# Optimization experiments

Hardware: AMD Instinct MI355X
Metric: run time of the kernel (lower is better)

The kernel has to match this reference:

```python
import jax, jax.numpy as jnp
import numpy as np
from jax import lax

RADIUS = 0.15
K = 32          # num_neighbors
S = 1024        # num_centers
GROUPS = 8      # GroupNorm groups
EPS = 1e-5


def furthest_point_sample(xyz, n_samples):
    # xyz: [B, N, 3] -> indices [B, n_samples] (sequential FPS, start at index 0)
    B, N, _ = xyz.shape
    def step(carry, _):
        min_d, far = carry                      # [B,N], [B]
        sel = jnp.take_along_axis(xyz, far[:, None, None], axis=1)  # [B,1,3]
        d = jnp.sum((xyz - sel) ** 2, axis=-1)  # [B,N]
        min_d = jnp.minimum(min_d, d)
        nxt = jnp.argmax(min_d, axis=-1).astype(jnp.int32)
        return (min_d, nxt), far
    init = (jnp.full((B, N), jnp.inf, dtype=xyz.dtype), jnp.zeros((B,), jnp.int32))
    _, idxs = lax.scan(step, init, None, length=n_samples)  # [n_samples, B]
    return idxs.T  # [B, n_samples]


def ball_query(centers, points, radius, k):
    # centers: [B,3,S], points: [B,3,N] -> neighbor indices [B,S,k]
    B = points.shape[0]
    N = points.shape[-1]
    d2 = jnp.sum((centers[:, :, :, None] - points[:, :, None, :]) ** 2, axis=1)  # [B,S,N]
    valid = d2 < radius * radius
    order = jnp.where(valid, jnp.arange(N, dtype=jnp.int32), jnp.int32(N))
    topk = jnp.sort(order, axis=-1)[..., :k]            # first-k in-ball indices (CUDA ball_query order)
    first = topk[..., :1]
    idx = jnp.where(topk < N, topk, first)              # pad shortfall with first in-ball point
    idx = jnp.where(idx == N, 0, idx)                   # empty ball -> index 0
    return idx


def grouping(x, idx):
    # x: [B,C,N], idx: [B,S,k] -> [B,C,S,k]
    B, C, N = x.shape
    _, s, k = idx.shape
    flat = idx.reshape(B, 1, s * k)
    g = jnp.take_along_axis(x, jnp.broadcast_to(flat, (B, C, s * k)), axis=2)
    return g.reshape(B, C, s, k)


def group_norm(x, gamma, beta):
    # x: [B,C,S,K], GroupNorm(GROUPS)
    B, C, s, k = x.shape
    xg = x.reshape(B, GROUPS, C // GROUPS, s, k)
    mu = jnp.mean(xg, axis=(2, 3, 4), keepdims=True)
    var = jnp.var(xg, axis=(2, 3, 4), keepdims=True)
    xn = ((xg - mu) * lax.rsqrt(var + EPS)).reshape(B, C, s, k)
    return xn * gamma[None, :, None, None] + beta[None, :, None, None]


def mlp_layer(x, w, b, gamma, beta):
    # 1x1 Conv2d + GroupNorm + swish; x: [B,C,S,K], w: [O,C]
    y = jnp.einsum('bcsk,oc->bosk', x, w) + b[None, :, None, None]
    y = group_norm(y, gamma, beta)
    return y * jax.nn.sigmoid(y)


def setup_inputs() -> dict:
    key = jax.random.key(0)
    ks = jax.random.split(key, 20)
    B, C_IN, N = 8, 128, 4096
    features = jax.random.normal(ks[0], (B, C_IN, N), jnp.float32)
    coords = jax.random.uniform(ks[1], (B, 3, N), jnp.float32)
    time_emb = jax.random.normal(ks[2], (B, 64, N), jnp.float32)
    style = jax.random.normal(ks[3], (B, 64), jnp.float32)
    chans = [C_IN + 3, 128, 128, 256]
    inp = dict(features=features, coords=coords, time_emb=time_emb, style=style)
    for i in range(3):
        ci, co = chans[i], chans[i + 1]
        inp[f'w{i+1}'] = jax.random.normal(ks[4 + 4 * i], (co, ci), jnp.float32) / np.sqrt(ci)
        inp[f'b{i+1}'] = jnp.zeros((co,), jnp.float32)
        inp[f'g{i+1}'] = jnp.ones((co,), jnp.float32)
        inp[f'be{i+1}'] = jnp.zeros((co,), jnp.float32)
    return inp


def reference(features, coords, time_emb, style,
              w1, b1, g1, be1, w2, b2, g2, be2, w3, b3, g3, be3):
    # FPS -> center coords
    fps_idx = furthest_point_sample(coords.transpose(0, 2, 1), S)       # [B,S]
    B = coords.shape[0]
    centers = jnp.take_along_axis(coords, jnp.broadcast_to(fps_idx[:, None, :], (B, 3, S)), axis=2)  # [B,3,S]
    # Ball query + grouping (include_coordinates=True)
    nidx = ball_query(centers, coords, RADIUS, K)                       # [B,S,K]
    ncoords = grouping(coords, nidx) - centers[:, :, :, None]           # [B,3,S,K]
    nfeat = jnp.concatenate([ncoords, grouping(features, nidx)], axis=1)  # [B,3+C,S,K]
    # SharedMLP (1x1 conv + GN(8) + swish) x3, then max over neighbors
    x = mlp_layer(nfeat, w1, b1, g1, be1)
    x = mlp_layer(x, w2, b2, g2, be2)
    x = mlp_layer(x, w3, b3, g3, be3)
    out = jnp.max(x, axis=-1)                                           # [B,256,S]
    return out, centers, time_emb[:, :, :S], style
```

## Files before the change

### kernel.cpp

```cpp
#include <hip/hip_runtime.h>
#include <hip/hip_bf16.h>

#define BATCH 8
#define NPTS 4096
#define NS   1024
#define NK   32
#define CIN  128
#define C1PAD 160
#define O1   128
#define O3   256
#define MTOT 32768
#define GN_EPS 1e-5f
#define SREP 64

typedef float f32x4 __attribute__((ext_vector_type(4)));
typedef float f32x2 __attribute__((ext_vector_type(2)));
typedef short s16x8 __attribute__((ext_vector_type(8)));
typedef short s16x4 __attribute__((ext_vector_type(4)));
typedef unsigned long long u64;
typedef u64 u64x2 __attribute__((ext_vector_type(2)));

static __device__ __forceinline__ unsigned short f2bf(float f){
  unsigned u = __float_as_uint(f);
  u += 0x7fffu + ((u >> 16) & 1u);
  return (unsigned short)(u >> 16);
}
static __device__ __forceinline__ float bf2f(unsigned short h){
  return __uint_as_float(((unsigned)h) << 16);
}
static __device__ __forceinline__ float exact_d2(float ax,float ay,float az,float bx,float by,float bz){
  float dx=__fadd_rn(ax,-bx), dy=__fadd_rn(ay,-by), dz=__fadd_rn(az,-bz);
  return __fadd_rn(__fadd_rn(__fmul_rn(dx,dx),__fmul_rn(dy,dy)),__fmul_rn(dz,dz));
}
static __device__ __forceinline__ unsigned wave_umax_dpp(unsigned v){
  unsigned o;
  o = (unsigned)__builtin_amdgcn_update_dpp(0, (int)v, 0x111, 0xf, 0xf, true); v = (o>v)?o:v;
  o = (unsigned)__builtin_amdgcn_update_dpp(0, (int)v, 0x112, 0xf, 0xf, true); v = (o>v)?o:v;
  o = (unsigned)__builtin_amdgcn_update_dpp(0, (int)v, 0x114, 0xf, 0xf, true); v = (o>v)?o:v;
  o = (unsigned)__builtin_amdgcn_update_dpp(0, (int)v, 0x118, 0xf, 0xf, true); v = (o>v)?o:v;
  o = (unsigned)__builtin_amdgcn_update_dpp(0, (int)v, 0x142, 0xf, 0xf, true); v = (o>v)?o:v;
  o = (unsigned)__builtin_amdgcn_update_dpp(0, (int)v, 0x143, 0xf, 0xf, true); v = (o>v)?o:v;
  return v;
}
static __device__ __forceinline__ float wave_fsum_dpp(float v){
  int o;
  o=__builtin_amdgcn_update_dpp(0,__float_as_int(v),0x111,0xf,0xf,true); v+=__int_as_float(o);
  o=__builtin_amdgcn_update_dpp(0,__float_as_int(v),0x112,0xf,0xf,true); v+=__int_as_float(o);
  o=__builtin_amdgcn_update_dpp(0,__float_as_int(v),0x114,0xf,0xf,true); v+=__int_as_float(o);
  o=__builtin_amdgcn_update_dpp(0,__float_as_int(v),0x118,0xf,0xf,true); v+=__int_as_float(o);
  o=__builtin_amdgcn_update_dpp(0,__float_as_int(v),0x142,0xf,0xf,true); v+=__int_as_float(o);
  o=__builtin_amdgcn_update_dpp(0,__float_as_int(v),0x143,0xf,0xf,true); v+=__int_as_float(o);
  return v;
}
static __device__ __forceinline__ float fast_sigmoid(float x){
  return __builtin_amdgcn_rcpf(1.0f + __expf(-x));
}
static __device__ __forceinline__ void stats_sum(const float* __restrict__ stats,
                                                 int layer,int b,int g,float& s1,float& s2){
  const float2* p = (const float2*)(stats + (size_t)(((layer*BATCH+b)*8+g)*SREP)*2);
  float a=0.f, q=0.f;
  #pragma unroll
  for(int r=0;r<SREP;++r){ float2 v=p[r]; a+=v.x; q+=v.y; }
  s1=a; s2=q;
}

#define FPS_BLOCKS 8
#define FT_BASE    8
#define FT_BLOCKS  128
#define ZP_BASE    136
#define ZP_BLOCKS  8
#define WP_BASE    144
#define WP_BLOCKS  130
#define MS_BASE    274
#define MS_BLOCKS  32
#define TOTAL_BLOCKS 306
#define WP_TASKS   (8704 + 3*BATCH*8*SREP*2)

__global__ __launch_bounds__(256) void k_fused(
    const float* __restrict__ coords, const float* __restrict__ features,
    const float* __restrict__ time_emb, const float* __restrict__ style,
    const float* __restrict__ w1, const float* __restrict__ w2, const float* __restrict__ w3,
    float* __restrict__ centers, float* __restrict__ out_time, float* __restrict__ out_style,
    unsigned short* __restrict__ featT, unsigned short* __restrict__ wfrag,
    float* __restrict__ stats){
  union U {
    struct { float4 lc[NPTS];
             unsigned long long red[2][4] __attribute__((aligned(16)));
             float cx_[NS]; float cy_[NS]; float cz_[NS]; } fps;
    float tile[64][65];
  };
  __shared__ U sm;
  const int blk = blockIdx.x;
  const int t = threadIdx.x;

  if(blk < FPS_BLOCKS){
    const int b = blk;
    const float* cb = coords + (size_t)b*3*NPTS;
    const int lane = t & 63, wid = t >> 6;
    f32x2 px2[8],py2[8],pz2[8],md2[8];
    #pragma unroll
    for(int i=0;i<8;++i){
      int p0 = t + (2*i)*256;
      px2[i]=(f32x2){cb[p0],cb[p0+256]};
      py2[i]=(f32x2){cb[NPTS+p0],cb[NPTS+p0+256]};
      pz2[i]=(f32x2){cb[2*NPTS+p0],cb[2*NPTS+p0+256]};
      md2[i]=(f32x2){3.4e38f,3.4e38f};
      sm.fps.lc[p0]     = make_float4(px2[i].x, py2[i].x, pz2[i].x, 0.f);
      sm.fps.lc[p0+256] = make_float4(px2[i].y, py2[i].y, pz2[i].y, 0.f);
    }
    float ax=cb[0], ay=cb[NPTS], az=cb[2*NPTS];
    if(t==0){ sm.fps.cx_[0]=ax; sm.fps.cy_[0]=ay; sm.fps.cz_[0]=az; }
    __syncthreads();
    for(int it=1; it<NS; ++it){
      {
        #pragma clang fp contract(off)
        f32x2 axv={ax,ax}, ayv={ay,ay}, azv={az,az};
        #pragma unroll
        for(int i=0;i<8;++i){
          f32x2 dx=px2[i]-axv, dy=py2[i]-ayv, dz=pz2[i]-azv;
          f32x2 d = dx*dx + dy*dy + dz*dz;
          md2[i]=__builtin_elementwise_min(md2[i],d);
        }
      }
      f32x2 t01=__builtin_elementwise_max(md2[0],md2[1]);
      f32x2 t23=__builtin_elementwise_max(md2[2],md2[3]);
      f32x2 t45=__builtin_elementwise_max(md2[4],md2[5]);
      f32x2 t67=__builtin_elementwise_max(md2[6],md2[7]);
      f32x2 ta=__builtin_elementwise_max(t01,t23);
      f32x2 tb=__builtin_elementwise_max(t45,t67);
      f32x2 tc=__builtin_elementwise_max(ta,tb);
      float bmax=fmaxf(tc.x,tc.y);
      unsigned bvb=(unsigned)__builtin_amdgcn_readlane((int)wave_umax_dpp(__float_as_uint(bmax)),63);
      unsigned cand=0u;
      #pragma unroll
      for(int s=15;s>=0;--s){
        float mv = (s&1)? md2[s>>1].y : md2[s>>1].x;
        cand = (__float_as_uint(mv)==bvb) ? ~(unsigned)(s*256+t) : cand;
      }
      unsigned mc = wave_umax_dpp(cand);
      const int buf=it&1;
      if(lane==63) sm.fps.red[buf][wid] = ((u64)bvb<<32) | mc;
      __syncthreads();
      u64x2 r0 = *(const u64x2*)&sm.fps.red[buf][0];
      u64x2 r1 = *(const u64x2*)&sm.fps.red[buf][2];
      u64 a0 = r0.x>r0.y?r0.x:r0.y;
      u64 a1 = r1.x>r1.y?r1.x:r1.y;
      u64 w  = a0>a1?a0:a1;
      unsigned idx = ~(unsigned)w;
      float4 c4 = sm.fps.lc[idx];
      ax=c4.x; ay=c4.y; az=c4.z;
      if(t==0){ sm.fps.cx_[it]=ax; sm.fps.cy_[it]=ay; sm.fps.cz_[it]=az; }
    }
    __syncthreads();
    for(int i=t;i<NS;i+=256){
      centers[(size_t)(b*3+0)*NS+i]=sm.fps.cx_[i];
      centers[(size_t)(b*3+1)*NS+i]=sm.fps.cy_[i];
      centers[(size_t)(b*3+2)*NS+i]=sm.fps.cz_[i];
    }
    return;
  }

  if(blk < ZP_BASE){
    const int pb = blk - FT_BASE;
    for(int j=0;j<8;++j){
      int tid = pb*8 + j;
      int bb = tid>>7, r = tid&127, ct = r>>6, pt = r&63;
      int c0 = ct*64, p0 = pt*64;
      #pragma unroll
      for(int i=0;i<16;++i){
        int c = (t>>6)*16 + i;
        sm.tile[c][t&63] = features[((size_t)bb*CIN + c0 + c)*NPTS + p0 + (t&63)];
      }
      __syncthreads();
      #pragma unroll
      for(int i=0;i<16;++i){
        int pl = (t>>6)*16 + i;
        featT[((size_t)bb*NPTS + p0 + pl)*C1PAD + c0 + (t&63)] = f2bf(sm.tile[t&63][pl]);
      }
      __syncthreads();
    }
    return;
  }

  if(blk < WP_BASE){
    const int zb = blk - ZP_BASE;
    s16x8 z = (s16x8){0,0,0,0,0,0,0,0};
    #pragma unroll 4
    for(int i=0;i<64;++i){
      int q = zb*16384 + i*256 + t;
      int bb = q>>14, rem = q&16383, r = rem>>2, c8 = (rem&3)*8;
      *(s16x8*)&featT[((size_t)bb*NPTS + r)*C1PAD + 128 + c8] = z;
    }
    return;
  }

  if(blk < MS_BASE){
    int task = (blk - WP_BASE)*256 + t;
    if(task >= WP_TASKS) return;
    if(task >= 8704){
      stats[task - 8704] = 0.f;
      return;
    }
    int layer, of, cs, ln, ncs; size_t base;
    if(task < 2560){ layer=0; ncs=5; base=0;     int r=task;      of=r/320; r%=320; cs=r>>6; ln=r&63; }
    else if(task < 4608){ layer=1; ncs=4; base=20480; int r=task-2560; of=r>>8; r&=255; cs=r>>6; ln=r&63; }
    else { layer=2; ncs=4; base=36864; int r=task-4608; of=r>>8; r&=255; cs=r>>6; ln=r&63; }
    int o = of*16 + (ln&15);
    s16x8 vals;
    #pragma unroll
    for(int i=0;i<8;++i){
      int c = cs*32 + (ln>>4)*8 + i;
      float v = 0.f;
      if(layer==0){
        if(c<128) v = w1[o*131 + c + 3];
        else if(c<131) v = w1[o*131 + (c-128)];
      } else if(layer==1){
        if(c<128) v = w2[o*128 + c];
      } else {
        if(c<128) v = w3[o*128 + c];
      }
      vals[i]=(short)f2bf(v);
    }
    *(s16x8*)&wfrag[base + ((size_t)(of*ncs + cs)*64 + ln)*8] = vals;
    return;
  }

  {
    const int mb = blk - MS_BASE;
    #pragma unroll 4
    for(int i=0;i<16;++i){
      int q = mb*4096 + i*256 + t;
      int f = q*4;
      int bb = f>>16, c = (f>>10)&63, s = f&1023;
      *(float4*)&out_time[f] = *(const float4*)&time_emb[((size_t)bb*64 + c)*NPTS + s];
    }
    if(mb==0){ out_style[t]=style[t]; out_style[256+t]=style[256+t]; }
  }
}

__global__ __launch_bounds__(256) void k_ballq(const float* __restrict__ coords,
                                               const float* __restrict__ centers,
                                               int* __restrict__ nidx){
  const int gw = (blockIdx.x*256 + threadIdx.x) >> 6;
  const int lane = threadIdx.x & 63;
  const int wl = (threadIdx.x >> 6);
  const int b = gw >> 10, s = gw & (NS-1);
  const float* cb = coords + (size_t)b*3*NPTS;
  const float cx = centers[(size_t)(b*3+0)*NS+s];
  const float cy = centers[(size_t)(b*3+1)*NS+s];
  const float cz = centers[(size_t)(b*3+2)*NS+s];
  __shared__ int slots[4][NK];
  int cnt = 0;
  for(int base=0; base<NPTS && cnt<NK; base+=64){
    int p = base + lane;
    float d2 = exact_d2(cb[p], cb[NPTS+p], cb[2*NPTS+p], cx,cy,cz);
    bool valid = d2 < 0.0225f;
    unsigned long long mask = __ballot(valid);
    int pos = cnt + (int)__popcll(mask & ((1ull<<lane)-1ull));
    if(valid && pos < NK) slots[wl][pos] = p;
    cnt += (int)__popcll(mask);
  }
  __syncthreads();
  int first = slots[wl][0];
  if(lane < NK){
    int v = (lane < cnt) ? slots[wl][lane] : first;
    nidx[((size_t)b*NS + s)*NK + lane] = v;
  }
}

__global__ __launch_bounds__(256) void k_gemm1(const unsigned short* __restrict__ featT,
    const int* __restrict__ nidx, const float* __restrict__ coords,
    const float* __restrict__ centers, const unsigned short* __restrict__ wfrag,
    const float* __restrict__ bias, unsigned short* __restrict__ yout,
    float* __restrict__ stats){
  const int b=blockIdx.y, mt=blockIdx.x;
  const int m0=mt*64;
  const int t=threadIdx.x, lane=t&63, wid=t>>6;
  __shared__ unsigned short xs[64][168];
  __shared__ unsigned short ys[64][136];
  __shared__ int pidx[64];
  __shared__ float cenS[2][3];
  __shared__ float wsum[2][8][4];
  if(t<64) pidx[t]=nidx[(size_t)b*MTOT + m0 + t];
  if(t>=64 && t<70){ int u=t-64; int j=u/3, c=u%3; cenS[j][c]=centers[((size_t)b*3+c)*NS + (m0>>5)+j]; }
  __syncthreads();
  for(int q=t;q<1280;q+=256){
    int r=q&63, ch=q>>6;
    *(s16x8*)&xs[r][ch*8] = *(const s16x8*)&featT[((size_t)b*NPTS + pidx[r])*C1PAD + ch*8];
  }
  __syncthreads();
  if(t<64){
    int p=pidx[t]; int sj=t>>5;
    float n0=__fadd_rn(coords[((size_t)b*3+0)*NPTS+p],-cenS[sj][0]);
    float n1=__fadd_rn(coords[((size_t)b*3+1)*NPTS+p],-cenS[sj][1]);
    float n2=__fadd_rn(coords[((size_t)b*3+2)*NPTS+p],-cenS[sj][2]);
    s16x4 nc={(short)f2bf(n0),(short)f2bf(n1),(short)f2bf(n2),0};
    *(s16x4*)&xs[t][128]=nc;
  }
  __syncthreads();
  f32x4 acc[8];
  #pragma unroll
  for(int i=0;i<8;++i) acc[i]=(f32x4){0.f,0.f,0.f,0.f};
  const unsigned short* xrow=&xs[wid*16+(lane&15)][0];
  #pragma unroll
  for(int cs=0;cs<5;++cs){
    s16x8 bfv=*(const s16x8*)&xrow[cs*32+(lane>>4)*8];
    #pragma unroll
    for(int of=0;of<8;++of){
      s16x8 afv=*(const s16x8*)&wfrag[((size_t)(of*5+cs)*64+lane)*8];
      acc[of]=__builtin_amdgcn_mfma_f32_16x16x32_bf16(afv,bfv,acc[of],0,0,0);
    }
  }
  #pragma unroll
  for(int of=0;of<8;++of){
    float ls=0.f,lq=0.f;
    int obase=of*16+((lane>>4)<<2);
    #pragma unroll
    for(int r=0;r<4;++r){
      float y=acc[of][r]+bias[obase+r];
      ys[wid*16+(lane&15)][obase+r]=f2bf(y);
      ls+=y; lq+=y*y;
    }
    ls=wave_fsum_dpp(ls); lq=wave_fsum_dpp(lq);
    if(lane==63){ wsum[0][of][wid]=ls; wsum[1][of][wid]=lq; }
  }
  __syncthreads();
  for(int q=t;q<1024;q+=256){
    int r=q&63, ch=q>>6;
    *(s16x8*)&yout[((size_t)b*MTOT+m0+r)*O1 + ch*8] = *(const s16x8*)&ys[r][ch*8];
  }
  if(t<8){
    float s1v=wsum[0][t][0]+wsum[0][t][1]+wsum[0][t][2]+wsum[0][t][3];
    float s2v=wsum[1][t][0]+wsum[1][t][1]+wsum[1][t][2]+wsum[1][t][3];
    int rep = mt & (SREP-1);
    atomicAdd(&stats[(((0*BATCH+b)*8+t)*SREP+rep)*2+0],s1v);
    atomicAdd(&stats[(((0*BATCH+b)*8+t)*SREP+rep)*2+1],s2v);
  }
}

template<int LAYER>
__global__ __launch_bounds__(256) void k_gemm23(const unsigned short* __restrict__ xin,
    const unsigned short* __restrict__ wfrag, const float* __restrict__ bias,
    const float* __restrict__ stats, const float* __restrict__ gprev,
    const float* __restrict__ beprev, unsigned short* __restrict__ yout,
    float* __restrict__ ymm, float* __restrict__ statsOut){
  const int b=blockIdx.y, mt=blockIdx.x;
  const int m0=mt*64;
  const int t=threadIdx.x, lane=t&63, wid=t>>6;
  __shared__ unsigned short xs[64][136];
  __shared__ unsigned short ys[64][136];
  __shared__ float lsc[CIN], lsh[CIN];
  __shared__ float wsum[2][8][4];
  if(t<CIN){
    int g = t>>4;
    const float cnt = 16.0f*NS*NK;
    float s1,s2; stats_sum(stats, LAYER-1, b, g, s1, s2);
    float mu=s1/cnt, var=s2/cnt-mu*mu;
    float sc=gprev[t]*rsqrtf(var+GN_EPS);
    lsc[t]=sc; lsh[t]=beprev[t]-mu*sc;
  }
  __syncthreads();
  for(int q=t;q<1024;q+=256){
    int r=q&63, ch=q>>6;
    s16x8 v = *(const s16x8*)&xin[((size_t)b*MTOT + m0 + r)*CIN + ch*8];
    s16x8 o;
    #pragma unroll
    for(int i=0;i<8;++i){
      int c=ch*8+i;
      float x = bf2f((unsigned short)v[i]);
      x = x*lsc[c] + lsh[c];
      o[i]=(short)f2bf(x*fast_sigmoid(x));
    }
    *(s16x8*)&xs[r][ch*8]=o;
  }
  __syncthreads();
  const unsigned short* xrow=&xs[wid*16+(lane&15)][0];
  s16x8 bfv[4];
  #pragma unroll
  for(int cs=0;cs<4;++cs) bfv[cs]=*(const s16x8*)&xrow[cs*32+(lane>>4)*8];
  const int NPH=(LAYER==2)?2:1;
  #pragma unroll
  for(int ph=0; ph<NPH; ++ph){
    f32x4 acc[8];
    #pragma unroll
    for(int i=0;i<8;++i) acc[i]=(f32x4){0.f,0.f,0.f,0.f};
    #pragma unroll
    for(int cs=0;cs<4;++cs){
      #pragma unroll
      for(int of=0;of<8;++of){
        int ofg=ph*8+of;
        s16x8 afv=*(const s16x8*)&wfrag[((size_t)(ofg*4+cs)*64+lane)*8];
        acc[of]=__builtin_amdgcn_mfma_f32_16x16x32_bf16(afv,bfv[cs],acc[of],0,0,0);
      }
    }
    #pragma unroll
    for(int of=0;of<8;++of){
      float ls=0.f,lq=0.f;
      int lobase=of*16+((lane>>4)<<2);
      #pragma unroll
      for(int r=0;r<4;++r){
        float y=acc[of][r]+bias[ph*128+lobase+r];
        ys[wid*16+(lane&15)][lobase+r]=f2bf(y);
        ls+=y; lq+=y*y;
      }
      ls=wave_fsum_dpp(ls); lq=wave_fsum_dpp(lq);
      if(lane==63){ wsum[0][of][wid]=ls; wsum[1][of][wid]=lq; }
    }
    __syncthreads();
    if constexpr(LAYER==1){
      for(int q=t;q<1024;q+=256){
        int r=q&63, ch=q>>6;
        *(s16x8*)&yout[((size_t)b*MTOT+m0+r)*O1 + ch*8] = *(const s16x8*)&ys[r][ch*8];
      }
    } else {
      int c = t&127, sg = t>>7;
      float mn=3.4e38f, mx=-3.4e38f;
      #pragma unroll 8
      for(int k=0;k<32;++k){
        float v = bf2f(ys[sg*32+k][c]);
        mn=fminf(mn,v); mx=fmaxf(mx,v);
      }
      *(float2*)&ymm[(((size_t)b*NS + mt*2 + sg)*512) + (size_t)(ph*128+c)*2] = make_float2(mn,mx);
    }
    if(t<8){
      float s1v=wsum[0][t][0]+wsum[0][t][1]+wsum[0][t][2]+wsum[0][t][3];
      float s2v=wsum[1][t][0]+wsum[1][t][1]+wsum[1][t][2]+wsum[1][t][3];
      int g = (LAYER==2) ? (ph*4 + (t>>1)) : t;
      int rep = mt & (SREP-1);
      atomicAdd(&statsOut[(((LAYER*BATCH+b)*8+g)*SREP+rep)*2+0],s1v);
      atomicAdd(&statsOut[(((LAYER*BATCH+b)*8+g)*SREP+rep)*2+1],s2v);
    }
    if(ph+1<NPH) __syncthreads();
  }
}

__global__ __launch_bounds__(256) void k_out(const float* __restrict__ ymm,
    const float* __restrict__ stats, const float* __restrict__ g3,
    const float* __restrict__ be3, float* __restrict__ out){
  const int b=blockIdx.z, st=blockIdx.x;
  const int t=threadIdx.x;
  __shared__ float outT[256][33];
  const int c=t, g=c>>5;
  const float cnt = 32.0f*NS*NK;
  float s1,s2; stats_sum(stats, 2, b, g, s1, s2);
  float mu=s1/cnt, var=s2/cnt-mu*mu;
  float sc=g3[c]*rsqrtf(var+GN_EPS);
  float sh=be3[c]-mu*sc;
  for(int si=0;si<32;++si){
    int s=st*32+si;
    float2 v=*(const float2*)&ymm[((size_t)b*NS+s)*512 + (size_t)c*2];
    float za=v.x*sc+sh, zb=v.y*sc+sh;
    float fa=za*fast_sigmoid(za);
    float fb=zb*fast_sigmoid(zb);
    outT[c][si]=fmaxf(fa,fb);
  }
  __syncthreads();
  #pragma unroll
  for(int i=0;i<32;++i){
    int row=(t>>5)+i*8;
    out[((size_t)(b*256+row))*NS + st*32 + (t&31)] = outT[row][t&31];
  }
}

extern "C" void kernel_launch(void* const* d_in, const int* in_sizes, int n_in,
                              void* d_out, int out_size, void* d_ws, size_t ws_size,
                              hipStream_t stream){
  const float* features=(const float*)d_in[0];
  const float* coords=(const float*)d_in[1];
  const float* time_emb=(const float*)d_in[2];
  const float* style=(const float*)d_in[3];
  const float* w1=(const float*)d_in[4];
  const float* b1=(const float*)d_in[5];
  const float* g1=(const float*)d_in[6];
  const float* be1=(const float*)d_in[7];
  const float* w2=(const float*)d_in[8];
  const float* b2=(const float*)d_in[9];
  const float* g2=(const float*)d_in[10];
  const float* be2=(const float*)d_in[11];
  const float* w3=(const float*)d_in[12];
  const float* b3=(const float*)d_in[13];
  const float* g3=(const float*)d_in[14];
  const float* be3=(const float*)d_in[15];

  float* out0=(float*)d_out;
  float* out_centers=out0 + (size_t)BATCH*O3*NS;
  float* out_time=out_centers + (size_t)BATCH*3*NS;
  float* out_style=out_time + (size_t)BATCH*64*NS;

  char* ws=(char*)d_ws;
  int* nidx=(int*)(ws + 131072);
  unsigned short* featT=(unsigned short*)(ws + 1179648);
  unsigned short* wfrag=(unsigned short*)(ws + 11796480);
  float* stats=(float*)(ws + 11939840);
  float* ymm=(float*)(ws + 12582912);
  unsigned short* y1=(unsigned short*)(ws + 33554432);
  unsigned short* y2=(unsigned short*)(ws + 100663296);

  k_fused<<<TOTAL_BLOCKS,256,0,stream>>>(coords,features,time_emb,style,w1,w2,w3,
                                         out_centers,out_time,out_style,featT,wfrag,stats);
  k_ballq<<<2048,256,0,stream>>>(coords,out_centers,nidx);
  k_gemm1<<<dim3(512,BATCH),256,0,stream>>>(featT,nidx,coords,out_centers,wfrag,b1,y1,stats);
  k_gemm23<1><<<dim3(512,BATCH),256,0,stream>>>(y1,wfrag+20480,b2,stats,g1,be1,y2,ymm,stats);
  k_gemm23<2><<<dim3(512,BATCH),256,0,stream>>>(y2,wfrag+36864,b3,stats,g2,be2,y2,ymm,stats);
  k_out<<<dim3(32,1,BATCH),256,0,stream>>>(ymm,stats,g3,be3,out0);
}
```

Measured before the change: 870.3 us.

## Overlap ball query and first GEMM with FPS via progress flags in fused kernel

The separate ball-query and layer-1 GEMM kernels are folded into the fused prologue kernel as 192 persistent blocks. FPS blocks publish centers directly to global memory and release a per-batch progress counter every 16 centers. The GEMM blocks spin on a prep-done counter and on that progress before doing the ball query and MFMA for each 64-row tile. This hides the serial FPS latency behind downstream work, but it relies on all 498 blocks being co-resident to avoid deadlock and adds spin-wait and atomic overhead.

```diff
diff --git a/kernel.cpp b/kernel.cpp
--- a/kernel.cpp
+++ b/kernel.cpp
@@ -73,21 +73,27 @@
 #define WP_BLOCKS  130
 #define MS_BASE    274
 #define MS_BLOCKS  32
-#define TOTAL_BLOCKS 306
+#define G1_BASE    306
+#define G1_BLOCKS  192
+#define TOTAL_BLOCKS 498
 #define WP_TASKS   (8704 + 3*BATCH*8*SREP*2)
+#define PREP_COUNT (FT_BLOCKS + ZP_BLOCKS + WP_BLOCKS)
 
 __global__ __launch_bounds__(256) void k_fused(
     const float* __restrict__ coords, const float* __restrict__ features,
     const float* __restrict__ time_emb, const float* __restrict__ style,
     const float* __restrict__ w1, const float* __restrict__ w2, const float* __restrict__ w3,
+    const float* __restrict__ b1,
     float* __restrict__ centers, float* __restrict__ out_time, float* __restrict__ out_style,
     unsigned short* __restrict__ featT, unsigned short* __restrict__ wfrag,
-    float* __restrict__ stats){
+    float* __restrict__ stats, unsigned short* __restrict__ y1,
+    int* __restrict__ prog, int* __restrict__ prep_done){
   union U {
     struct { float4 lc[NPTS];
-             unsigned long long red[2][4] __attribute__((aligned(16)));
-             float cx_[NS]; float cy_[NS]; float cz_[NS]; } fps;
+             unsigned long long red[2][4] __attribute__((aligned(16))); } fps;
     float tile[64][65];
+    struct { unsigned short xs[64][168]; unsigned short ys[64][136];
+             int pidx[64]; float cenS[2][3]; float wsum[2][8][4]; } g1;
   };
   __shared__ U sm;
   const int blk = blockIdx.x;
@@ -109,7 +115,11 @@
       sm.fps.lc[p0+256] = make_float4(px2[i].y, py2[i].y, pz2[i].y, 0.f);
     }
     float ax=cb[0], ay=cb[NPTS], az=cb[2*NPTS];
-    if(t==0){ sm.fps.cx_[0]=ax; sm.fps.cy_[0]=ay; sm.fps.cz_[0]=az; }
+    if(t==0){
+      centers[(size_t)(b*3+0)*NS]=ax;
+      centers[(size_t)(b*3+1)*NS]=ay;
+      centers[(size_t)(b*3+2)*NS]=az;
+    }
     __syncthreads();
     for(int it=1; it<NS; ++it){
       {
@@ -149,13 +159,15 @@
       unsigned idx = ~(unsigned)w;
       float4 c4 = sm.fps.lc[idx];
       ax=c4.x; ay=c4.y; az=c4.z;
-      if(t==0){ sm.fps.cx_[it]=ax; sm.fps.cy_[it]=ay; sm.fps.cz_[it]=az; }
-    }
-    __syncthreads();
-    for(int i=t;i<NS;i+=256){
-      centers[(size_t)(b*3+0)*NS+i]=sm.fps.cx_[i];
-      centers[(size_t)(b*3+1)*NS+i]=sm.fps.cy_[i];
-      centers[(size_t)(b*3+2)*NS+i]=sm.fps.cz_[i];
+      if(t==0){
+        centers[(size_t)(b*3+0)*NS+it]=ax;
+        centers[(size_t)(b*3+1)*NS+it]=ay;
+        centers[(size_t)(b*3+2)*NS+it]=az;
+        if((it&15)==15){
+          __threadfence();
+          __hip_atomic_store(&prog[b], it+1, __ATOMIC_RELEASE, __HIP_MEMORY_SCOPE_AGENT);
+        }
+      }
     }
     return;
   }
@@ -179,6 +191,9 @@
       }
       __syncthreads();
     }
+    __threadfence();
+    __syncthreads();
+    if(t==0) __hip_atomic_fetch_add(prep_done,1,__ATOMIC_RELEASE,__HIP_MEMORY_SCOPE_AGENT);
     return;
   }
 
@@ -191,41 +206,48 @@
       int bb = q>>14, rem = q&16383, r = rem>>2, c8 = (rem&3)*8;
       *(s16x8*)&featT[((size_t)bb*NPTS + r)*C1PAD + 128 + c8] = z;
     }
+    __threadfence();
+    __syncthreads();
+    if(t==0) __hip_atomic_fetch_add(prep_done,1,__ATOMIC_RELEASE,__HIP_MEMORY_SCOPE_AGENT);
     return;
   }
 
   if(blk < MS_BASE){
     int task = (blk - WP_BASE)*256 + t;
-    if(task >= WP_TASKS) return;
-    if(task >= 8704){
-      stats[task - 8704] = 0.f;
-      return;
-    }
-    int layer, of, cs, ln, ncs; size_t base;
-    if(task < 2560){ layer=0; ncs=5; base=0;     int r=task;      of=r/320; r%=320; cs=r>>6; ln=r&63; }
-    else if(task < 4608){ layer=1; ncs=4; base=20480; int r=task-2560; of=r>>8; r&=255; cs=r>>6; ln=r&63; }
-    else { layer=2; ncs=4; base=36864; int r=task-4608; of=r>>8; r&=255; cs=r>>6; ln=r&63; }
-    int o = of*16 + (ln&15);
-    s16x8 vals;
-    #pragma unroll
-    for(int i=0;i<8;++i){
-      int c = cs*32 + (ln>>4)*8 + i;
-      float v = 0.f;
-      if(layer==0){
-        if(c<128) v = w1[o*131 + c + 3];
-        else if(c<131) v = w1[o*131 + (c-128)];
-      } else if(layer==1){
-        if(c<128) v = w2[o*128 + c];
+    if(task < WP_TASKS){
+      if(task >= 8704){
+        stats[task - 8704] = 0.f;
       } else {
-        if(c<128) v = w3[o*128 + c];
-      }
-      vals[i]=(short)f2bf(v);
-    }
-    *(s16x8*)&wfrag[base + ((size_t)(of*ncs + cs)*64 + ln)*8] = vals;
+        int layer, of, cs, ln, ncs; size_t base;
+        if(task < 2560){ layer=0; ncs=5; base=0;     int r=task;      of=r/320; r%=320; cs=r>>6; ln=r&63; }
+        else if(task < 4608){ layer=1; ncs=4; base=20480; int r=task-2560; of=r>>8; r&=255; cs=r>>6; ln=r&63; }
+        else { layer=2; ncs=4; base=36864; int r=task-4608; of=r>>8; r&=255; cs=r>>6; ln=r&63; }
+        int o = of*16 + (ln&15);
+        s16x8 vals;
+        #pragma unroll
+        for(int i=0;i<8;++i){
+          int c = cs*32 + (ln>>4)*8 + i;
+          float v = 0.f;
+          if(layer==0){
+            if(c<128) v = w1[o*131 + c + 3];
+            else if(c<131) v = w1[o*131 + (c-128)];
+          } else if(layer==1){
+            if(c<128) v = w2[o*128 + c];
+          } else {
+            if(c<128) v = w3[o*128 + c];
+          }
+          vals[i]=(short)f2bf(v);
+        }
+        *(s16x8*)&wfrag[base + ((size_t)(of*ncs + cs)*64 + ln)*8] = vals;
+      }
+    }
+    __threadfence();
+    __syncthreads();
+    if(t==0) __hip_atomic_fetch_add(prep_done,1,__ATOMIC_RELEASE,__HIP_MEMORY_SCOPE_AGENT);
     return;
   }
 
-  {
+  if(blk < G1_BASE){
     const int mb = blk - MS_BASE;
     #pragma unroll 4
     for(int i=0;i<16;++i){
@@ -235,106 +257,97 @@
       *(float4*)&out_time[f] = *(const float4*)&time_emb[((size_t)bb*64 + c)*NPTS + s];
     }
     if(mb==0){ out_style[t]=style[t]; out_style[256+t]=style[256+t]; }
-  }
-}
-
-__global__ __launch_bounds__(256) void k_ballq(const float* __restrict__ coords,
-                                               const float* __restrict__ centers,
-                                               int* __restrict__ nidx){
-  const int gw = (blockIdx.x*256 + threadIdx.x) >> 6;
-  const int lane = threadIdx.x & 63;
-  const int wl = (threadIdx.x >> 6);
-  const int b = gw >> 10, s = gw & (NS-1);
-  const float* cb = coords + (size_t)b*3*NPTS;
-  const float cx = centers[(size_t)(b*3+0)*NS+s];
-  const float cy = centers[(size_t)(b*3+1)*NS+s];
-  const float cz = centers[(size_t)(b*3+2)*NS+s];
-  __shared__ int slots[4][NK];
-  int cnt = 0;
-  for(int base=0; base<NPTS && cnt<NK; base+=64){
-    int p = base + lane;
-    float d2 = exact_d2(cb[p], cb[NPTS+p], cb[2*NPTS+p], cx,cy,cz);
-    bool valid = d2 < 0.0225f;
-    unsigned long long mask = __ballot(valid);
-    int pos = cnt + (int)__popcll(mask & ((1ull<<lane)-1ull));
-    if(valid && pos < NK) slots[wl][pos] = p;
-    cnt += (int)__popcll(mask);
-  }
-  __syncthreads();
-  int first = slots[wl][0];
-  if(lane < NK){
-    int v = (lane < cnt) ? slots[wl][lane] : first;
-    nidx[((size_t)b*NS + s)*NK + lane] = v;
-  }
-}
-
-__global__ __launch_bounds__(256) void k_gemm1(const unsigned short* __restrict__ featT,
-    const int* __restrict__ nidx, const float* __restrict__ coords,
-    const float* __restrict__ centers, const unsigned short* __restrict__ wfrag,
-    const float* __restrict__ bias, unsigned short* __restrict__ yout,
-    float* __restrict__ stats){
-  const int b=blockIdx.y, mt=blockIdx.x;
-  const int m0=mt*64;
-  const int t=threadIdx.x, lane=t&63, wid=t>>6;
-  __shared__ unsigned short xs[64][168];
-  __shared__ unsigned short ys[64][136];
-  __shared__ int pidx[64];
-  __shared__ float cenS[2][3];
-  __shared__ float wsum[2][8][4];
-  if(t<64) pidx[t]=nidx[(size_t)b*MTOT + m0 + t];
-  if(t>=64 && t<70){ int u=t-64; int j=u/3, c=u%3; cenS[j][c]=centers[((size_t)b*3+c)*NS + (m0>>5)+j]; }
-  __syncthreads();
-  for(int q=t;q<1280;q+=256){
-    int r=q&63, ch=q>>6;
-    *(s16x8*)&xs[r][ch*8] = *(const s16x8*)&featT[((size_t)b*NPTS + pidx[r])*C1PAD + ch*8];
-  }
-  __syncthreads();
-  if(t<64){
-    int p=pidx[t]; int sj=t>>5;
-    float n0=__fadd_rn(coords[((size_t)b*3+0)*NPTS+p],-cenS[sj][0]);
-    float n1=__fadd_rn(coords[((size_t)b*3+1)*NPTS+p],-cenS[sj][1]);
-    float n2=__fadd_rn(coords[((size_t)b*3+2)*NPTS+p],-cenS[sj][2]);
-    s16x4 nc={(short)f2bf(n0),(short)f2bf(n1),(short)f2bf(n2),0};
-    *(s16x4*)&xs[t][128]=nc;
-  }
-  __syncthreads();
-  f32x4 acc[8];
-  #pragma unroll
-  for(int i=0;i<8;++i) acc[i]=(f32x4){0.f,0.f,0.f,0.f};
-  const unsigned short* xrow=&xs[wid*16+(lane&15)][0];
-  #pragma unroll
-  for(int cs=0;cs<5;++cs){
-    s16x8 bfv=*(const s16x8*)&xrow[cs*32+(lane>>4)*8];
-    #pragma unroll
-    for(int of=0;of<8;++of){
-      s16x8 afv=*(const s16x8*)&wfrag[((size_t)(of*5+cs)*64+lane)*8];
-      acc[of]=__builtin_amdgcn_mfma_f32_16x16x32_bf16(afv,bfv,acc[of],0,0,0);
-    }
-  }
-  #pragma unroll
-  for(int of=0;of<8;++of){
-    float ls=0.f,lq=0.f;
-    int obase=of*16+((lane>>4)<<2);
-    #pragma unroll
-    for(int r=0;r<4;++r){
-      float y=acc[of][r]+bias[obase+r];
-      ys[wid*16+(lane&15)][obase+r]=f2bf(y);
-      ls+=y; lq+=y*y;
-    }
-    ls=wave_fsum_dpp(ls); lq=wave_fsum_dpp(lq);
-    if(lane==63){ wsum[0][of][wid]=ls; wsum[1][of][wid]=lq; }
-  }
-  __syncthreads();
-  for(int q=t;q<1024;q+=256){
-    int r=q&63, ch=q>>6;
-    *(s16x8*)&yout[((size_t)b*MTOT+m0+r)*O1 + ch*8] = *(const s16x8*)&ys[r][ch*8];
-  }
-  if(t<8){
-    float s1v=wsum[0][t][0]+wsum[0][t][1]+wsum[0][t][2]+wsum[0][t][3];
-    float s2v=wsum[1][t][0]+wsum[1][t][1]+wsum[1][t][2]+wsum[1][t][3];
-    int rep = mt & (SREP-1);
-    atomicAdd(&stats[(((0*BATCH+b)*8+t)*SREP+rep)*2+0],s1v);
-    atomicAdd(&stats[(((0*BATCH+b)*8+t)*SREP+rep)*2+1],s2v);
+    return;
+  }
+
+  {
+    const int brel = blk - G1_BASE;
+    const int lane=t&63, wid=t>>6;
+    while(__hip_atomic_load(prep_done,__ATOMIC_ACQUIRE,__HIP_MEMORY_SCOPE_AGENT) < PREP_COUNT)
+      __builtin_amdgcn_s_sleep(2);
+    for(int tid=brel; tid<4096; tid+=G1_BLOCKS){
+      const int b = tid&7, mt = tid>>3, m0 = mt*64;
+      const int need = 2*mt+2;
+      while(__hip_atomic_load(&prog[b],__ATOMIC_ACQUIRE,__HIP_MEMORY_SCOPE_AGENT) < need)
+        __builtin_amdgcn_s_sleep(2);
+      if(wid<2){
+        const int s0=(m0>>5)+wid;
+        const float cx=centers[(size_t)(b*3+0)*NS+s0];
+        const float cy=centers[(size_t)(b*3+1)*NS+s0];
+        const float cz=centers[(size_t)(b*3+2)*NS+s0];
+        if(lane==0){ sm.g1.cenS[wid][0]=cx; sm.g1.cenS[wid][1]=cy; sm.g1.cenS[wid][2]=cz; }
+        const float* cb=coords+(size_t)b*3*NPTS;
+        int cnt=0;
+        for(int base=0;base<NPTS&&cnt<NK;base+=64){
+          int p=base+lane;
+          float d2=exact_d2(cb[p],cb[NPTS+p],cb[2*NPTS+p],cx,cy,cz);
+          bool valid=d2<0.0225f;
+          unsigned long long mask=__ballot(valid);
+          int pos=cnt+(int)__popcll(mask&((1ull<<lane)-1ull));
+          if(valid&&pos<NK) sm.g1.pidx[wid*32+pos]=p;
+          cnt+=(int)__popcll(mask);
+        }
+        int first=sm.g1.pidx[wid*32];
+        if(lane<NK){
+          int v=(lane<cnt)?sm.g1.pidx[wid*32+lane]:first;
+          sm.g1.pidx[wid*32+lane]=v;
+        }
+      }
+      __syncthreads();
+      for(int q=t;q<1280;q+=256){
+        int r=q&63, ch=q>>6;
+        *(s16x8*)&sm.g1.xs[r][ch*8] = *(const s16x8*)&featT[((size_t)b*NPTS + sm.g1.pidx[r])*C1PAD + ch*8];
+      }
+      __syncthreads();
+      if(t<64){
+        int p=sm.g1.pidx[t]; int sj=t>>5;
+        float n0=__fadd_rn(coords[((size_t)b*3+0)*NPTS+p],-sm.g1.cenS[sj][0]);
+        float n1=__fadd_rn(coords[((size_t)b*3+1)*NPTS+p],-sm.g1.cenS[sj][1]);
+        float n2=__fadd_rn(coords[((size_t)b*3+2)*NPTS+p],-sm.g1.cenS[sj][2]);
+        s16x4 nc={(short)f2bf(n0),(short)f2bf(n1),(short)f2bf(n2),0};
+        *(s16x4*)&sm.g1.xs[t][128]=nc;
+      }
+      __syncthreads();
+      f32x4 acc[8];
+      #pragma unroll
+      for(int i=0;i<8;++i) acc[i]=(f32x4){0.f,0.f,0.f,0.f};
+      const unsigned short* xrow=&sm.g1.xs[wid*16+(lane&15)][0];
+      #pragma unroll
+      for(int cs=0;cs<5;++cs){
+        s16x8 bfv=*(const s16x8*)&xrow[cs*32+(lane>>4)*8];
+        #pragma unroll
+        for(int of=0;of<8;++of){
+          s16x8 afv=*(const s16x8*)&wfrag[((size_t)(of*5+cs)*64+lane)*8];
+          acc[of]=__builtin_amdgcn_mfma_f32_16x16x32_bf16(afv,bfv,acc[of],0,0,0);
+        }
+      }
+      #pragma unroll
+      for(int of=0;of<8;++of){
+        float ls=0.f,lq=0.f;
+        int obase=of*16+((lane>>4)<<2);
+        #pragma unroll
+        for(int r=0;r<4;++r){
+          float y=acc[of][r]+b1[obase+r];
+          sm.g1.ys[wid*16+(lane&15)][obase+r]=f2bf(y);
+          ls+=y; lq+=y*y;
+        }
+        ls=wave_fsum_dpp(ls); lq=wave_fsum_dpp(lq);
+        if(lane==63){ sm.g1.wsum[0][of][wid]=ls; sm.g1.wsum[1][of][wid]=lq; }
+      }
+      __syncthreads();
+      for(int q=t;q<1024;q+=256){
+        int r=q&63, ch=q>>6;
+        *(s16x8*)&y1[((size_t)b*MTOT+m0+r)*O1 + ch*8] = *(const s16x8*)&sm.g1.ys[r][ch*8];
+      }
+      if(t<8){
+        float s1v=sm.g1.wsum[0][t][0]+sm.g1.wsum[0][t][1]+sm.g1.wsum[0][t][2]+sm.g1.wsum[0][t][3];
+        float s2v=sm.g1.wsum[1][t][0]+sm.g1.wsum[1][t][1]+sm.g1.wsum[1][t][2]+sm.g1.wsum[1][t][3];
+        int rep = mt & (SREP-1);
+        atomicAdd(&stats[(((0*BATCH+b)*8+t)*SREP+rep)*2+0],s1v);
+        atomicAdd(&stats[(((0*BATCH+b)*8+t)*SREP+rep)*2+1],s2v);
+      }
+      __syncthreads();
+    }
   }
 }
 
@@ -488,18 +501,18 @@
   float* out_style=out_time + (size_t)BATCH*64*NS;
 
   char* ws=(char*)d_ws;
-  int* nidx=(int*)(ws + 131072);
   unsigned short* featT=(unsigned short*)(ws + 1179648);
   unsigned short* wfrag=(unsigned short*)(ws + 11796480);
+  int* ctr=(int*)(ws + 11935744);
   float* stats=(float*)(ws + 11939840);
   float* ymm=(float*)(ws + 12582912);
   unsigned short* y1=(unsigned short*)(ws + 33554432);
   unsigned short* y2=(unsigned short*)(ws + 100663296);
 
-  k_fused<<<TOTAL_BLOCKS,256,0,stream>>>(coords,features,time_emb,style,w1,w2,w3,
-                                         out_centers,out_time,out_style,featT,wfrag,stats);
-  k_ballq<<<2048,256,0,stream>>>(coords,out_centers,nidx);
-  k_gemm1<<<dim3(512,BATCH),256,0,stream>>>(featT,nidx,coords,out_centers,wfrag,b1,y1,stats);
+  hipMemsetAsync(ctr, 0, 64, stream);
+  k_fused<<<TOTAL_BLOCKS,256,0,stream>>>(coords,features,time_emb,style,w1,w2,w3,b1,
+                                         out_centers,out_time,out_style,featT,wfrag,stats,y1,
+                                         ctr,ctr+8);
   k_gemm23<1><<<dim3(512,BATCH),256,0,stream>>>(y1,wfrag+20480,b2,stats,g1,be1,y2,ymm,stats);
   k_gemm23<2><<<dim3(512,BATCH),256,0,stream>>>(y2,wfrag+36864,b3,stats,g2,be2,y2,ymm,stats);
   k_out<<<dim3(32,1,BATCH),256,0,stream>>>(ymm,stats,g3,be3,out0);
```

Result: slower. 890.5 us (+2.3%).
